# Kernel optimization log

Hardware: AMD Instinct MI355X
Metric: run time of the kernel (lower is better)

The kernel has to match this reference:

```python
import jax, jax.numpy as jnp
import numpy as np

LN_EPS = 1e-5
IH_IDX = np.array([0, 2, 4, 6])  # layernorm_iih, fih, aih, oih
HH_IDX = np.array([1, 3, 5, 7])  # layernorm_ihh, fhh, ahh, ohh


def _ln(x, g, b):
    # LayerNorm over last dim, matching nn.LayerNorm(hidden_size)
    mu = jnp.mean(x, axis=-1, keepdims=True)
    xc = x - mu
    var = jnp.mean(xc * xc, axis=-1, keepdims=True)
    return g * xc * jax.lax.rsqrt(var + LN_EPS) + b


def setup_inputs() -> dict:
    B, I, H = 4096, 1024, 1024
    key = jax.random.key(0)
    ks = jax.random.split(key, 8)
    stdv = 1.0 / np.sqrt(H)  # reset_parameters: uniform(-stdv, stdv)
    return {
        "x": jax.random.normal(ks[0], (B, I), jnp.float32),
        "h": jax.random.normal(ks[1], (B, H), jnp.float32),
        "c": jax.random.normal(ks[2], (B, H), jnp.float32),
        "w_ih": jax.random.uniform(ks[3], (4 * H, I), jnp.float32, -stdv, stdv),
        "w_hh": jax.random.uniform(ks[4], (4 * H, H), jnp.float32, -stdv, stdv),
        "b_ih": jax.random.uniform(ks[5], (4 * H,), jnp.float32, -stdv, stdv),
        # 9 LayerNorms stacked: [iih, ihh, fih, fhh, aih, ahh, oih, ohh, ct]
        "ln_gamma": 1.0 + 0.1 * jax.random.normal(ks[6], (9, H), jnp.float32),
        "ln_beta": 0.1 * jax.random.normal(ks[7], (9, H), jnp.float32),
        "time": 0,
    }


def reference(x, h, c, w_ih, w_hh, b_ih, ln_gamma, ln_beta, time):
    B = x.shape[0]
    H = w_hh.shape[1]
    # pre-activations, split into the 4 gates (i, f, a, o) along dim 1
    pre_ih = (x @ w_ih.T).reshape(B, 4, H)   # [B,4,H]
    pre_hh = (h @ w_hh.T).reshape(B, 4, H)   # [B,4,H]
    # per-gate LayerNorm on ih and hh contributions, then add bias
    gates = (
        _ln(pre_ih, ln_gamma[IH_IDX], ln_beta[IH_IDX])
        + _ln(pre_hh, ln_gamma[HH_IDX], ln_beta[HH_IDX])
        + b_ih.reshape(4, H)
    )
    i, f, a, o = gates[:, 0], gates[:, 1], gates[:, 2], gates[:, 3]
    c_new = jax.nn.sigmoid(f) * c + jax.nn.sigmoid(i) * jnp.tanh(a)
    h_new = jax.nn.sigmoid(o) * jnp.tanh(_ln(c_new, ln_gamma[8], ln_beta[8]))
    return (h_new, c_new)
```

## Files before the change

kernel.cpp:

```cpp
#include <hip/hip_runtime.h>
#include <hip/hip_bf16.h>
#include <stdint.h>


#define HDIM 1024
#define BATCH 4096
#define NGATE 4096
#define KDIM 1024

typedef __bf16 bf16x8 __attribute__((ext_vector_type(8)));
typedef float f32x4 __attribute__((ext_vector_type(4)));
typedef unsigned short ushort8_t __attribute__((ext_vector_type(8)));

__device__ __forceinline__ unsigned short f2bf(float f) {
  unsigned int u = __builtin_bit_cast(unsigned int, f);
  unsigned int r = (u + 0x7fffu + ((u >> 16) & 1u)) >> 16;
  return (unsigned short)r;
}

__device__ __forceinline__ float bf2f(unsigned short s) {
  unsigned int u = ((unsigned int)s) << 16;
  return __builtin_bit_cast(float, u);
}

__device__ __forceinline__ void gl_lds16(const void* g, void* l) {
  __builtin_amdgcn_global_load_lds(
      (__attribute__((address_space(1))) unsigned int*)g,
      (__attribute__((address_space(3))) unsigned int*)l,
      16, 0, 0);
}

#define BAR() asm volatile("s_barrier" ::: "memory")
#define WAITL() asm volatile("s_waitcnt lgkmcnt(0)" ::: "memory")
#define WAITV(N) asm volatile("s_waitcnt vmcnt(" #N ")" ::: "memory")

__global__ __launch_bounds__(256) void cast_bf16_kernel(
    const float* __restrict__ x, const float* __restrict__ h,
    const float* __restrict__ wi, const float* __restrict__ wh,
    unsigned short* __restrict__ xb, unsigned short* __restrict__ hb,
    unsigned short* __restrict__ wib, unsigned short* __restrict__ whb) {
  const float* src;
  unsigned short* dst;
  switch (blockIdx.y) {
    case 0: src = x;  dst = xb;  break;
    case 1: src = h;  dst = hb;  break;
    case 2: src = wi; dst = wib; break;
    default: src = wh; dst = whb; break;
  }
  size_t i = ((size_t)blockIdx.x * 256 + threadIdx.x) * 4;
  float4 v = *(const float4*)(src + i);
  ushort4 o;
  o.x = f2bf(v.x); o.y = f2bf(v.y); o.z = f2bf(v.z); o.w = f2bf(v.w);
  *(ushort4*)(dst + i) = o;
}

__global__ __launch_bounds__(512, 2) void gemm_bt_kernel(
    const unsigned short* __restrict__ A0p, const unsigned short* __restrict__ B0p,
    unsigned short* __restrict__ C0p,
    const unsigned short* __restrict__ A1p, const unsigned short* __restrict__ B1p,
    unsigned short* __restrict__ C1p) {
  const unsigned short* A = blockIdx.z ? A1p : A0p;
  const unsigned short* B = blockIdx.z ? B1p : B0p;
  unsigned short* C = blockIdx.z ? C1p : C0p;

  __shared__ alignas(16) unsigned short As[4 * 128 * 64];
  __shared__ alignas(16) unsigned short Bs[4 * 128 * 64];

  const int tid = threadIdx.x;
  const int wave = tid >> 6;
  const int lane = tid & 63;
  const int wr = wave >> 2;
  const int wc = wave & 3;
  const int bm = blockIdx.x * 256;
  const int bn = blockIdx.y * 256;

  const int srow = lane >> 3;
  const int scol = ((lane & 7) ^ (lane >> 3)) * 8;
  const int m15 = lane & 15;
  const int quad = lane >> 4;
  const int sw = m15 & 7;

  f32x4 acc[8][4];
#pragma unroll
  for (int i = 0; i < 8; ++i)
#pragma unroll
    for (int j = 0; j < 4; ++j)
#pragma unroll
      for (int r = 0; r < 4; ++r) acc[i][j][r] = 0.0f;

  auto stage = [&](const unsigned short* __restrict__ G, int grow0, int kk,
                   unsigned short* slot) {
    gl_lds16(G + (size_t)(grow0 + wave * 8 + srow) * KDIM + kk + scol,
             slot + wave * 8 * 64);
    gl_lds16(G + (size_t)(grow0 + 64 + wave * 8 + srow) * KDIM + kk + scol,
             slot + (64 + wave * 8) * 64);
  };

  stage(A, bm,       0,  &As[0]);
  stage(B, bn,       0,  &Bs[0]);
  stage(A, bm + 128, 0,  &As[1 * 8192]);
  stage(B, bn + 128, 0,  &Bs[1 * 8192]);
  stage(A, bm,       64, &As[2 * 8192]);
  stage(B, bn,       64, &Bs[2 * 8192]);
  WAITV(8);
  BAR();

  for (int t = 0; t < 16; ++t) {
    const int p2  = (t & 1) * 2;
    const int n2  = ((t + 1) & 1) * 2;
    const int kk1 = ((t + 1) & 15) * 64;
    const int kk2 = ((t + 2) & 15) * 64;

#pragma unroll
    for (int q = 0; q < 4; ++q) {
      const int h = q >> 1;
      const int g = q & 1;

      bf16x8 af[4][2], bfr[2][2];
      const unsigned short* Abase = &As[(p2 + h) * 8192];
      const unsigned short* Bbase = &Bs[(p2 + g) * 8192];
#pragma unroll
      for (int i2 = 0; i2 < 4; ++i2) {
        int r = wr * 64 + i2 * 16 + m15;
#pragma unroll
        for (int s = 0; s < 2; ++s)
          af[i2][s] = *(const bf16x8*)&Abase[r * 64 + (((s * 4 + quad) ^ sw) << 3)];
      }
#pragma unroll
      for (int j2 = 0; j2 < 2; ++j2) {
        int r = wc * 32 + j2 * 16 + m15;
#pragma unroll
        for (int s = 0; s < 2; ++s)
          bfr[j2][s] = *(const bf16x8*)&Bbase[r * 64 + (((s * 4 + quad) ^ sw) << 3)];
      }

      if (q == 0)      stage(A, bm + 128, kk1, &As[(n2 + 1) * 8192]);
      else if (q == 1) stage(B, bn + 128, kk1, &Bs[(n2 + 1) * 8192]);
      else if (q == 2) stage(A, bm,       kk2, &As[p2 * 8192]);
      else             stage(B, bn,       kk2, &Bs[p2 * 8192]);

      BAR();
      WAITL();
      __builtin_amdgcn_s_setprio(1);
#pragma unroll
      for (int i2 = 0; i2 < 4; ++i2)
#pragma unroll
        for (int j2 = 0; j2 < 2; ++j2) {
          acc[h * 4 + i2][g * 2 + j2] = __builtin_amdgcn_mfma_f32_16x16x32_bf16(
              af[i2][0], bfr[j2][0], acc[h * 4 + i2][g * 2 + j2], 0, 0, 0);
          acc[h * 4 + i2][g * 2 + j2] = __builtin_amdgcn_mfma_f32_16x16x32_bf16(
              af[i2][1], bfr[j2][1], acc[h * 4 + i2][g * 2 + j2], 0, 0, 0);
        }
      __builtin_amdgcn_s_setprio(0);
      if (q == 0) WAITV(6);
      if (q == 3) WAITV(8);
      BAR();
    }
  }
  WAITV(0);

#pragma unroll
  for (int i = 0; i < 8; ++i) {
    int m = bm + (i >> 2) * 128 + wr * 64 + (i & 3) * 16 + quad * 4;
#pragma unroll
    for (int j = 0; j < 4; ++j) {
      int n = bn + (j >> 1) * 128 + wc * 32 + (j & 1) * 16 + m15;
#pragma unroll
      for (int rr = 0; rr < 4; ++rr)
        C[(size_t)(m + rr) * NGATE + n] = f2bf(acc[i][j][rr]);
    }
  }
}

__device__ __forceinline__ float fast_sigmoid(float x) {
  return __builtin_amdgcn_rcpf(1.0f + __expf(-x));
}
__device__ __forceinline__ float fast_tanh(float x) {
  return 1.0f - 2.0f * __builtin_amdgcn_rcpf(__expf(2.0f * x) + 1.0f);
}

__global__ __launch_bounds__(256) void ln_gate_kernel(
    const unsigned short* __restrict__ pih, const unsigned short* __restrict__ phh,
    const float* __restrict__ c, const float* __restrict__ b_ih,
    const float* __restrict__ gamma, const float* __restrict__ beta,
    float* __restrict__ h_out, float* __restrict__ c_out) {
  __shared__ float lds[32];
  const int b = blockIdx.x;
  const int t = threadIdx.x;
  const int wave = t >> 6;
  const int lane = t & 63;
  const float inv_h = 1.0f / 1024.0f;
  const float eps = 1e-5f;

  {
    const size_t rb = (size_t)b * NGATE + wave * HDIM + lane * 16;
    ushort8_t a0 = *(const ushort8_t*)&pih[rb];
    ushort8_t a1 = *(const ushort8_t*)&pih[rb + 8];
    ushort8_t e0 = *(const ushort8_t*)&phh[rb];
    ushort8_t e1 = *(const ushort8_t*)&phh[rb + 8];
    float s0 = 0.f, q0 = 0.f, s1 = 0.f, q1 = 0.f;
#pragma unroll
    for (int r = 0; r < 8; ++r) {
      float va = bf2f(a0[r]), vb = bf2f(a1[r]);
      float ea = bf2f(e0[r]), eb = bf2f(e1[r]);
      s0 += va + vb; q0 += va * va + vb * vb;
      s1 += ea + eb; q1 += ea * ea + eb * eb;
    }
#pragma unroll
    for (int o = 1; o < 64; o <<= 1) {
      s0 += __shfl_xor(s0, o, 64); q0 += __shfl_xor(q0, o, 64);
      s1 += __shfl_xor(s1, o, 64); q1 += __shfl_xor(q1, o, 64);
    }
    if (lane == 0) {
      float mu0 = s0 * inv_h;
      float mu1 = s1 * inv_h;
      lds[wave * 4 + 0] = mu0;
      lds[wave * 4 + 1] = rsqrtf(q0 * inv_h - mu0 * mu0 + eps);
      lds[wave * 4 + 2] = mu1;
      lds[wave * 4 + 3] = rsqrtf(q1 * inv_h - mu1 * mu1 + eps);
    }
  }
  __syncthreads();

  const int j = t * 4;
  float gate[4][4];
#pragma unroll
  for (int g = 0; g < 4; ++g) {
    float mu0 = lds[g * 4 + 0], rs0 = lds[g * 4 + 1];
    float mu1 = lds[g * 4 + 2], rs1 = lds[g * 4 + 3];
    ushort4 a4 = *(const ushort4*)&pih[(size_t)b * NGATE + g * HDIM + j];
    ushort4 e4 = *(const ushort4*)&phh[(size_t)b * NGATE + g * HDIM + j];
    float vih[4] = {bf2f(a4.x), bf2f(a4.y), bf2f(a4.z), bf2f(a4.w)};
    float vhh[4] = {bf2f(e4.x), bf2f(e4.y), bf2f(e4.z), bf2f(e4.w)};
    float4 g0 = *(const float4*)&gamma[(2 * g) * HDIM + j];
    float4 b0 = *(const float4*)&beta[(2 * g) * HDIM + j];
    float4 g1 = *(const float4*)&gamma[(2 * g + 1) * HDIM + j];
    float4 b1 = *(const float4*)&beta[(2 * g + 1) * HDIM + j];
    float4 bb = *(const float4*)&b_ih[g * HDIM + j];
    const float* g0p = &g0.x; const float* b0p = &b0.x;
    const float* g1p = &g1.x; const float* b1p = &b1.x;
    const float* bbp = &bb.x;
#pragma unroll
    for (int r = 0; r < 4; ++r) {
      float gih = g0p[r] * ((vih[r] - mu0) * rs0) + b0p[r];
      float ghh = g1p[r] * ((vhh[r] - mu1) * rs1) + b1p[r];
      gate[g][r] = gih + ghh + bbp[r];
    }
  }

  float4 cv4 = *(const float4*)&c[(size_t)b * HDIM + j];
  const float* cvp = &cv4.x;
  float cn[4], ov[4];
  float s2 = 0.f, q2 = 0.f;
#pragma unroll
  for (int r = 0; r < 4; ++r) {
    float iv = fast_sigmoid(gate[0][r]);
    float fv = fast_sigmoid(gate[1][r]);
    float av = fast_tanh(gate[2][r]);
    ov[r] = fast_sigmoid(gate[3][r]);
    float cvn = fv * cvp[r] + iv * av;
    cn[r] = cvn;
    s2 += cvn; q2 += cvn * cvn;
  }
#pragma unroll
  for (int o = 1; o < 64; o <<= 1) {
    s2 += __shfl_xor(s2, o, 64);
    q2 += __shfl_xor(q2, o, 64);
  }
  __syncthreads();
  if (lane == 0) { lds[16 + wave * 2] = s2; lds[16 + wave * 2 + 1] = q2; }
  __syncthreads();
  s2 = lds[16] + lds[18] + lds[20] + lds[22];
  q2 = lds[17] + lds[19] + lds[21] + lds[23];
  float mu = s2 * inv_h;
  float rs = rsqrtf(q2 * inv_h - mu * mu + eps);

  float4 g8 = *(const float4*)&gamma[8 * HDIM + j];
  float4 b8 = *(const float4*)&beta[8 * HDIM + j];
  const float* g8p = &g8.x; const float* b8p = &b8.x;
  float4 ho, co;
  float* hop = &ho.x; float* cop = &co.x;
#pragma unroll
  for (int r = 0; r < 4; ++r) {
    float ln = g8p[r] * ((cn[r] - mu) * rs) + b8p[r];
    hop[r] = ov[r] * fast_tanh(ln);
    cop[r] = cn[r];
  }
  *(float4*)&h_out[(size_t)b * HDIM + j] = ho;
  *(float4*)&c_out[(size_t)b * HDIM + j] = co;
}

extern "C" void kernel_launch(void* const* d_in, const int* in_sizes, int n_in,
                              void* d_out, int out_size, void* d_ws, size_t ws_size,
                              hipStream_t stream) {
  const float* x     = (const float*)d_in[0];
  const float* h     = (const float*)d_in[1];
  const float* c     = (const float*)d_in[2];
  const float* w_ih  = (const float*)d_in[3];
  const float* w_hh  = (const float*)d_in[4];
  const float* b_ih  = (const float*)d_in[5];
  const float* gamma = (const float*)d_in[6];
  const float* beta  = (const float*)d_in[7];

  char* ws = (char*)d_ws;
  unsigned short* xb  = (unsigned short*)(ws);
  unsigned short* hb  = (unsigned short*)(ws + (size_t)8 * 1024 * 1024);
  unsigned short* wib = (unsigned short*)(ws + (size_t)16 * 1024 * 1024);
  unsigned short* whb = (unsigned short*)(ws + (size_t)24 * 1024 * 1024);
  unsigned short* pih = (unsigned short*)(ws + (size_t)32 * 1024 * 1024);
  unsigned short* phh = (unsigned short*)(ws + (size_t)64 * 1024 * 1024);

  dim3 cgrid(4096, 4, 1);
  cast_bf16_kernel<<<cgrid, 256, 0, stream>>>(x, h, w_ih, w_hh, xb, hb, wib, whb);

  dim3 ggrid(16, 16, 2);
  gemm_bt_kernel<<<ggrid, 512, 0, stream>>>(xb, wib, pih, hb, whb, phh);

  float* h_out = (float*)d_out;
  float* c_out = h_out + (size_t)BATCH * HDIM;
  ln_gate_kernel<<<4096, 256, 0, stream>>>(pih, phh, c, b_ih, gamma, beta, h_out, c_out);
}
```

Baseline: 260.7 us.

## Restructure GEMM main loop to reuse LDS fragments across quadrants and reorder staging

The bf16 MFMA GEMM main loop now loads A and B fragments once per k-step and reuses them across the four output quadrants (A0·B0, A0·B1, A1·B1, A1·B0), instead of reloading both operands for every quadrant. The prefetch schedule changes from two k-steps ahead to one k-step ahead, with a new order of staged halves and adjusted vmcnt waits. Global pointers for each wave are precomputed to cut address arithmetic. This reduces LDS read traffic but holds more fragment registers live and shortens the prefetch distance, which may expose more global-load latency.

```diff
diff --git a/kernel.cpp b/kernel.cpp
--- a/kernel.cpp
+++ b/kernel.cpp
@@ -80,6 +80,9 @@
   const int quad = lane >> 4;
   const int sw = m15 & 7;
 
+  const unsigned short* gwA = A + (size_t)(bm + wave * 8 + srow) * KDIM + scol;
+  const unsigned short* gwB = B + (size_t)(bn + wave * 8 + srow) * KDIM + scol;
+
   f32x4 acc[8][4];
 #pragma unroll
   for (int i = 0; i < 8; ++i)
@@ -88,74 +91,123 @@
 #pragma unroll
       for (int r = 0; r < 4; ++r) acc[i][j][r] = 0.0f;
 
-  auto stage = [&](const unsigned short* __restrict__ G, int grow0, int kk,
-                   unsigned short* slot) {
-    gl_lds16(G + (size_t)(grow0 + wave * 8 + srow) * KDIM + kk + scol,
-             slot + wave * 8 * 64);
-    gl_lds16(G + (size_t)(grow0 + 64 + wave * 8 + srow) * KDIM + kk + scol,
-             slot + (64 + wave * 8) * 64);
+  auto stage = [&](const unsigned short* gw, int goff, int kk, unsigned short* slot) {
+    gl_lds16(gw + (size_t)goff * KDIM + kk, slot + wave * 512);
+    gl_lds16(gw + (size_t)(goff + 64) * KDIM + kk, slot + wave * 512 + 4096);
   };
 
-  stage(A, bm,       0,  &As[0]);
-  stage(B, bn,       0,  &Bs[0]);
-  stage(A, bm + 128, 0,  &As[1 * 8192]);
-  stage(B, bn + 128, 0,  &Bs[1 * 8192]);
-  stage(A, bm,       64, &As[2 * 8192]);
-  stage(B, bn,       64, &Bs[2 * 8192]);
-  WAITV(8);
+  stage(gwA, 0,   0, &As[0]);
+  stage(gwB, 0,   0, &Bs[0]);
+  stage(gwB, 128, 0, &Bs[1 * 8192]);
+  stage(gwA, 128, 0, &As[1 * 8192]);
+  WAITV(4);
   BAR();
 
   for (int t = 0; t < 16; ++t) {
     const int p2  = (t & 1) * 2;
     const int n2  = ((t + 1) & 1) * 2;
     const int kk1 = ((t + 1) & 15) * 64;
-    const int kk2 = ((t + 2) & 15) * 64;
-
-#pragma unroll
-    for (int q = 0; q < 4; ++q) {
-      const int h = q >> 1;
-      const int g = q & 1;
-
-      bf16x8 af[4][2], bfr[2][2];
-      const unsigned short* Abase = &As[(p2 + h) * 8192];
-      const unsigned short* Bbase = &Bs[(p2 + g) * 8192];
-#pragma unroll
-      for (int i2 = 0; i2 < 4; ++i2) {
-        int r = wr * 64 + i2 * 16 + m15;
-#pragma unroll
-        for (int s = 0; s < 2; ++s)
-          af[i2][s] = *(const bf16x8*)&Abase[r * 64 + (((s * 4 + quad) ^ sw) << 3)];
+
+    const unsigned short* A0b = &As[p2 * 8192];
+    const unsigned short* A1b = &As[(p2 + 1) * 8192];
+    const unsigned short* B0b = &Bs[p2 * 8192];
+    const unsigned short* B1b = &Bs[(p2 + 1) * 8192];
+
+    bf16x8 af[4][2], b0[2][2], b1[2][2];
+
+#pragma unroll
+    for (int i2 = 0; i2 < 4; ++i2) {
+      int r = wr * 64 + i2 * 16 + m15;
+#pragma unroll
+      for (int s = 0; s < 2; ++s)
+        af[i2][s] = *(const bf16x8*)&A0b[r * 64 + (((s * 4 + quad) ^ sw) << 3)];
+    }
+#pragma unroll
+    for (int j2 = 0; j2 < 2; ++j2) {
+      int r = wc * 32 + j2 * 16 + m15;
+#pragma unroll
+      for (int s = 0; s < 2; ++s)
+        b0[j2][s] = *(const bf16x8*)&B0b[r * 64 + (((s * 4 + quad) ^ sw) << 3)];
+    }
+    stage(gwA, 0, kk1, &As[n2 * 8192]);
+    BAR();
+    WAITL();
+    __builtin_amdgcn_s_setprio(1);
+#pragma unroll
+    for (int i2 = 0; i2 < 4; ++i2)
+#pragma unroll
+      for (int j2 = 0; j2 < 2; ++j2) {
+        acc[i2][j2] = __builtin_amdgcn_mfma_f32_16x16x32_bf16(
+            af[i2][0], b0[j2][0], acc[i2][j2], 0, 0, 0);
+        acc[i2][j2] = __builtin_amdgcn_mfma_f32_16x16x32_bf16(
+            af[i2][1], b0[j2][1], acc[i2][j2], 0, 0, 0);
       }
+    __builtin_amdgcn_s_setprio(0);
+    WAITV(4);
+    BAR();
+
+#pragma unroll
+    for (int j2 = 0; j2 < 2; ++j2) {
+      int r = wc * 32 + j2 * 16 + m15;
+#pragma unroll
+      for (int s = 0; s < 2; ++s)
+        b1[j2][s] = *(const bf16x8*)&B1b[r * 64 + (((s * 4 + quad) ^ sw) << 3)];
+    }
+    stage(gwB, 0, kk1, &Bs[n2 * 8192]);
+    BAR();
+    WAITL();
+    __builtin_amdgcn_s_setprio(1);
+#pragma unroll
+    for (int i2 = 0; i2 < 4; ++i2)
 #pragma unroll
       for (int j2 = 0; j2 < 2; ++j2) {
-        int r = wc * 32 + j2 * 16 + m15;
-#pragma unroll
-        for (int s = 0; s < 2; ++s)
-          bfr[j2][s] = *(const bf16x8*)&Bbase[r * 64 + (((s * 4 + quad) ^ sw) << 3)];
+        acc[i2][2 + j2] = __builtin_amdgcn_mfma_f32_16x16x32_bf16(
+            af[i2][0], b1[j2][0], acc[i2][2 + j2], 0, 0, 0);
+        acc[i2][2 + j2] = __builtin_amdgcn_mfma_f32_16x16x32_bf16(
+            af[i2][1], b1[j2][1], acc[i2][2 + j2], 0, 0, 0);
       }
-
-      if (q == 0)      stage(A, bm + 128, kk1, &As[(n2 + 1) * 8192]);
-      else if (q == 1) stage(B, bn + 128, kk1, &Bs[(n2 + 1) * 8192]);
-      else if (q == 2) stage(A, bm,       kk2, &As[p2 * 8192]);
-      else             stage(B, bn,       kk2, &Bs[p2 * 8192]);
-
-      BAR();
-      WAITL();
-      __builtin_amdgcn_s_setprio(1);
-#pragma unroll
-      for (int i2 = 0; i2 < 4; ++i2)
-#pragma unroll
-        for (int j2 = 0; j2 < 2; ++j2) {
-          acc[h * 4 + i2][g * 2 + j2] = __builtin_amdgcn_mfma_f32_16x16x32_bf16(
-              af[i2][0], bfr[j2][0], acc[h * 4 + i2][g * 2 + j2], 0, 0, 0);
-          acc[h * 4 + i2][g * 2 + j2] = __builtin_amdgcn_mfma_f32_16x16x32_bf16(
-              af[i2][1], bfr[j2][1], acc[h * 4 + i2][g * 2 + j2], 0, 0, 0);
-        }
-      __builtin_amdgcn_s_setprio(0);
-      if (q == 0) WAITV(6);
-      if (q == 3) WAITV(8);
-      BAR();
-    }
+    __builtin_amdgcn_s_setprio(0);
+    WAITV(4);
+    BAR();
+
+#pragma unroll
+    for (int i2 = 0; i2 < 4; ++i2) {
+      int r = wr * 64 + i2 * 16 + m15;
+#pragma unroll
+      for (int s = 0; s < 2; ++s)
+        af[i2][s] = *(const bf16x8*)&A1b[r * 64 + (((s * 4 + quad) ^ sw) << 3)];
+    }
+    stage(gwB, 128, kk1, &Bs[(n2 + 1) * 8192]);
+    BAR();
+    WAITL();
+    __builtin_amdgcn_s_setprio(1);
+#pragma unroll
+    for (int i2 = 0; i2 < 4; ++i2)
+#pragma unroll
+      for (int j2 = 0; j2 < 2; ++j2) {
+        acc[4 + i2][2 + j2] = __builtin_amdgcn_mfma_f32_16x16x32_bf16(
+            af[i2][0], b1[j2][0], acc[4 + i2][2 + j2], 0, 0, 0);
+        acc[4 + i2][2 + j2] = __builtin_amdgcn_mfma_f32_16x16x32_bf16(
+            af[i2][1], b1[j2][1], acc[4 + i2][2 + j2], 0, 0, 0);
+      }
+    __builtin_amdgcn_s_setprio(0);
+    BAR();
+
+    stage(gwA, 128, kk1, &As[(n2 + 1) * 8192]);
+    BAR();
+    __builtin_amdgcn_s_setprio(1);
+#pragma unroll
+    for (int i2 = 0; i2 < 4; ++i2)
+#pragma unroll
+      for (int j2 = 0; j2 < 2; ++j2) {
+        acc[4 + i2][j2] = __builtin_amdgcn_mfma_f32_16x16x32_bf16(
+            af[i2][0], b0[j2][0], acc[4 + i2][j2], 0, 0, 0);
+        acc[4 + i2][j2] = __builtin_amdgcn_mfma_f32_16x16x32_bf16(
+            af[i2][1], b0[j2][1], acc[4 + i2][j2], 0, 0, 0);
+      }
+    __builtin_amdgcn_s_setprio(0);
+    WAITV(4);
+    BAR();
   }
   WAITV(0);
 
```

Measured after the change: 242.7 us. 1.07x faster.
